# Kernel optimization log

Hardware: AMD Instinct MI355X
Metric: run time of the kernel (lower is better)

Reference implementation:

```python
import jax, jax.numpy as jnp
import numpy as np

# RootMLP architecture constants (data_size=16, width=64, depth=2, in=1, out=2*data)
DATA = 16
WIDTH = 64
OUT = 2 * DATA
LAYER_SHAPES = [(WIDTH, 1), (WIDTH,), (WIDTH, WIDTH), (WIDTH,), (OUT, WIDTH), (OUT,)]
SIZES = [int(np.prod(s)) for s in LAYER_SHAPES]
OFFS = np.cumsum([0] + SIZES).tolist()
LATENT = OFFS[-1]  # 6368


def _mlp_apply(thet, x):
    # Unflatten latent vector into MLP weights (order: W0,b0,W1,b1,W2,b2) and run it.
    W0 = thet[OFFS[0]:OFFS[1]].reshape(WIDTH, 1)
    b0 = thet[OFFS[1]:OFFS[2]]
    W1 = thet[OFFS[2]:OFFS[3]].reshape(WIDTH, WIDTH)
    b1 = thet[OFFS[3]:OFFS[4]]
    W2 = thet[OFFS[4]:OFFS[5]].reshape(OUT, WIDTH)
    b2 = thet[OFFS[5]:OFFS[6]]
    h = jax.nn.relu(W0 @ x + b0)
    h = jax.nn.relu(W1 @ h + b1)
    return W2 @ h + b2  # (OUT,)


def setup_inputs() -> dict:
    key = jax.random.key(0)
    k1, k2, k3, k4 = jax.random.split(key, 4)
    batch, T = 8, 64
    xs = jax.random.normal(k1, (batch, T, DATA), dtype=jnp.float32)
    ts = jnp.tile(jnp.linspace(0.0, 1.0, T, dtype=jnp.float32), (batch, 1))
    # A initialized as identity in the source; tiny noise keeps the recurrence non-trivial yet stable.
    A = jnp.eye(LATENT, dtype=jnp.float32) + 1e-4 * jax.random.normal(k2, (LATENT, LATENT), dtype=jnp.float32)
    B = 0.01 * jax.random.normal(k3, (LATENT, DATA + 1), dtype=jnp.float32)
    theta0 = 0.05 * jax.random.normal(k4, (LATENT,), dtype=jnp.float32)
    return {"xs": xs, "ts": ts, "A": A, "B": B, "theta0": theta0}


def reference(xs, ts, A, B, theta0):
    # xs: (batch, T, DATA); ts: (batch, T)
    def forward(xs_, ts_):
        def f(carry, inp):
            thet, x_hat, x_prev, t_prev = carry
            x_true, t_curr = inp  # x_true: (DATA,), t_curr: (1,)
            delta_t = t_curr - t_prev
            # forcing_prob = 1.0  ->  bernoulli(key, 1.0) is always True -> teacher forcing
            x_t = x_true
            # time_as_channel=True: prepend time to both current and previous inputs
            xt_c = jnp.concatenate([t_curr, x_t])
            xp_c = jnp.concatenate([t_prev, x_prev])
            thet_next = A @ thet + B @ (xt_c - xp_c)
            root_in = t_curr + delta_t  # (1,)
            out = _mlp_apply(thet_next, root_in)  # (2*DATA,)
            mean = jnp.tanh(out[:DATA])
            std = jax.nn.softplus(jnp.tanh(out[DATA:]))  # apply_tanh_uncertainty=True
            x_next = jnp.concatenate([mean, std])
            # carry update per source: new x_hat = mean, new x_prev = old x_hat
            return (thet_next, mean, x_hat, t_curr), x_next

        init = (theta0, xs_[0], xs_[0], -ts_[1:2])
        _, ys = jax.lax.scan(f, init, (xs_, ts_[:, None]))
        return ys  # (T, 2*DATA)

    return jax.vmap(forward)(xs, ts)
```

## Files before the change

kernel.cpp:

```cpp
#include <hip/hip_runtime.h>
#include <hip/hip_bf16.h>
#include <cmath>

#define LATENT 6368
#define TSTEPS 64
#define NDATA 16
#define NPANEL 398
#define KSPLIT 8
#define NCHUNK 199
#define CPS 25
#define NTILE (NPANEL*KSPLIT)
#define KBLK 796
#define AGENT __HIP_MEMORY_SCOPE_AGENT

typedef __attribute__((ext_vector_type(8))) short short8v;
typedef __attribute__((ext_vector_type(4))) float floatx4;

__device__ __forceinline__ unsigned short f2bf(float x) {
    union { float f; unsigned u; } c; c.f = x;
    unsigned r = (c.u + 0x7FFFu + ((c.u >> 16) & 1u)) >> 16;
    return (unsigned short)r;
}
__device__ __forceinline__ float bf2f(unsigned short h) {
    union { unsigned u; float f; } c; c.u = ((unsigned)h) << 16; return c.f;
}

__device__ __forceinline__ unsigned long long ld64c(const void* p) {
    return __hip_atomic_load((const unsigned long long*)p, __ATOMIC_RELAXED, AGENT);
}
__device__ __forceinline__ short8v ldT16c(const unsigned short* p) {
    union { short8v v; unsigned long long q[2]; } r;
    r.q[0] = ld64c(p);
    r.q[1] = ld64c(p + 4);
    return r.v;
}
__device__ __forceinline__ float ldfc(const float* p) {
    return __hip_atomic_load(p, __ATOMIC_RELAXED, AGENT);
}
__device__ __forceinline__ void stfc(float* p, float v) {
    __hip_atomic_store(p, v, __ATOMIC_RELAXED, AGENT);
}
__device__ __forceinline__ void stu16c(unsigned short* p, unsigned short v) {
    __hip_atomic_store(p, v, __ATOMIC_RELAXED, AGENT);
}

__global__ __launch_bounds__(64) void row_scale(const float* __restrict__ A,
                                                float* __restrict__ S) {
    int row = blockIdx.x;
    int lane = threadIdx.x;
    const float* Ar = A + (size_t)row * LATENT;
    float m = 0.f;
    for (int i = 0; i < 25; ++i) {
        int idx = i * 256 + lane * 4;
        if (idx + 4 <= LATENT) {
            float4 v = *reinterpret_cast<const float4*>(Ar + idx);
            float a0 = v.x - (idx + 0 == row ? 1.f : 0.f);
            float a1 = v.y - (idx + 1 == row ? 1.f : 0.f);
            float a2 = v.z - (idx + 2 == row ? 1.f : 0.f);
            float a3 = v.w - (idx + 3 == row ? 1.f : 0.f);
            m = fmaxf(m, fmaxf(fmaxf(fabsf(a0), fabsf(a1)), fmaxf(fabsf(a2), fabsf(a3))));
        }
    }
#pragma unroll
    for (int o = 32; o; o >>= 1) m = fmaxf(m, __shfl_xor(m, o, 64));
    if (lane == 0) S[row] = fmaxf(m, 1e-30f) * (1.0f / 32767.0f);
}

__global__ __launch_bounds__(256) void convert_Eq(const float* __restrict__ A,
                                                  const float* __restrict__ S,
                                                  short* __restrict__ Eq,
                                                  int total) {
    int t = blockIdx.x * 256 + threadIdx.x;
    if (t >= total) return;
    int row = t / KBLK;
    int kb  = t - row * KBLK;
    const float4* src = reinterpret_cast<const float4*>(A + (size_t)row * LATENT + kb * 8);
    float4 v0 = src[0];
    float4 v1 = src[1];
    float v[8] = {v0.x, v0.y, v0.z, v0.w, v1.x, v1.y, v1.z, v1.w};
    int jd = row - kb * 8;
    if (jd >= 0 && jd < 8) v[jd] -= 1.0f;
    float inv = 1.0f / S[row];
    union { short8v s; short q[8]; } o;
#pragma unroll
    for (int j = 0; j < 8; ++j) {
        float qf = rintf(v[j] * inv);
        qf = fminf(fmaxf(qf, -32767.f), 32767.f);
        o.q[j] = (short)qf;
    }
    int p = row >> 4, rowl = row & 15, c = kb >> 2, kgrp = kb & 3;
    int lane = kgrp * 16 + rowl;
    *reinterpret_cast<short8v*>(Eq + ((size_t)(p * NCHUNK + c)) * 512 + lane * 8) = o.s;
}

__global__ __launch_bounds__(256) void init_theta(const float* __restrict__ th0,
                                                  float* __restrict__ T0,
                                                  unsigned short* __restrict__ TTA) {
    int r = blockIdx.x * blockDim.x + threadIdx.x;
    if (r >= LATENT) return;
    float v = th0[r];
#pragma unroll
    for (int b = 0; b < 8; ++b) T0[r * 8 + b] = v;
    unsigned short hb = f2bf(v);
    unsigned short lb = f2bf(v - bf2f(hb));
#pragma unroll
    for (int n = 0; n < 8; ++n) {
        TTA[n * LATENT + r] = hb;
        TTA[(n + 8) * LATENT + r] = lb;
    }
}

__device__ void mlp_batch(const float* __restrict__ Tcur, const float* __restrict__ ts,
                          float* __restrict__ mwrite, float* __restrict__ ys,
                          int i, int b, int lane) {
    float tc = ts[b * TSTEPS + i];
    float tp = (i == 0) ? -ts[b * TSTEPS + 1] : ts[b * TSTEPS + i - 1];
    float rin = 2.f * tc - tp;
    float h0 = fmaxf(Tcur[(size_t)lane * 8 + b] * rin + Tcur[(size_t)(64 + lane) * 8 + b], 0.f);
    float h1 = Tcur[(size_t)(4224 + lane) * 8 + b];
#pragma unroll 8
    for (int k = 0; k < 64; ++k)
        h1 += Tcur[(size_t)(128 + lane * 64 + k) * 8 + b] * __shfl(h0, k, 64);
    h1 = fmaxf(h1, 0.f);
    float o = 0.f;
    if (lane < 32) o = Tcur[(size_t)(6336 + lane) * 8 + b];
#pragma unroll 8
    for (int k = 0; k < 64; ++k) {
        float hk = __shfl(h1, k, 64);
        if (lane < 32) o += Tcur[(size_t)(4288 + lane * 64 + k) * 8 + b] * hk;
    }
    if (lane < 32) {
        float z = tanhf(o);
        float res;
        if (lane < 16) { res = z; mwrite[b * NDATA + lane] = z; }
        else           { res = log1pf(expf(z)); }
        ys[(size_t)b * (TSTEPS * 32) + (size_t)i * 32 + lane] = res;
    }
}

__device__ void mlp_batch_coh(const float* __restrict__ Tcur, const float* __restrict__ ts,
                              float* __restrict__ mwrite, float* __restrict__ ys,
                              int i, int b, int lane) {
    float tc = ts[b * TSTEPS + i];
    float tp = (i == 0) ? -ts[b * TSTEPS + 1] : ts[b * TSTEPS + i - 1];
    float rin = 2.f * tc - tp;
    float h0 = fmaxf(ldfc(&Tcur[(size_t)lane * 8 + b]) * rin
                     + ldfc(&Tcur[(size_t)(64 + lane) * 8 + b]), 0.f);
    float h1 = ldfc(&Tcur[(size_t)(4224 + lane) * 8 + b]);
#pragma unroll 8
    for (int k = 0; k < 64; ++k)
        h1 += ldfc(&Tcur[(size_t)(128 + lane * 64 + k) * 8 + b]) * __shfl(h0, k, 64);
    h1 = fmaxf(h1, 0.f);
    float o = 0.f;
    if (lane < 32) o = ldfc(&Tcur[(size_t)(6336 + lane) * 8 + b]);
#pragma unroll 8
    for (int k = 0; k < 64; ++k) {
        float hk = __shfl(h1, k, 64);
        if (lane < 32) o += ldfc(&Tcur[(size_t)(4288 + lane * 64 + k) * 8 + b]) * hk;
    }
    if (lane < 32) {
        float z = tanhf(o);
        float res;
        if (lane < 16) { res = z; stfc(&mwrite[b * NDATA + lane], z); }
        else           { res = log1pf(expf(z)); }
        ys[(size_t)b * (TSTEPS * 32) + (size_t)i * 32 + lane] = res;
    }
}

__device__ __forceinline__ void gsync2(unsigned* grpCnt, unsigned* superCnt,
                                       unsigned* gEpoch, unsigned iter) {
    asm volatile("s_waitcnt vmcnt(0)" ::: "memory");
    __syncthreads();
    if (threadIdx.x == 0) {
        unsigned g = blockIdx.x & 15u;
        unsigned gsz = (g < 8u) ? 13u : 12u;
        unsigned v = __hip_atomic_fetch_add(&grpCnt[g * 32], 1u, __ATOMIC_RELAXED, AGENT);
        if (v == iter * gsz - 1u) {
            unsigned w = __hip_atomic_fetch_add(superCnt, 1u, __ATOMIC_RELAXED, AGENT);
            if (w == iter * 16u - 1u) {
#pragma unroll
                for (int i2 = 0; i2 < 16; ++i2)
                    __hip_atomic_store(&gEpoch[i2 * 32], iter, __ATOMIC_RELAXED, AGENT);
            }
        }
        while (__hip_atomic_load(&gEpoch[g * 32], __ATOMIC_RELAXED, AGENT) < iter)
            __builtin_amdgcn_s_sleep(4);
    }
    __syncthreads();
}

#define COMP(EV, TP) do {                                                       \
    union { short8v sv; unsigned short us[8]; } EHu, ELu;                       \
    _Pragma("unroll")                                                           \
    for (int j = 0; j < 8; ++j) {                                               \
        int q = (EV)[j];                                                        \
        union { float f; unsigned u; } ch, cl;                                  \
        ch.f = (float)(q >> 8);                                                 \
        cl.f = (float)(q & 255);                                                \
        EHu.us[j] = (unsigned short)(ch.u >> 16);                               \
        ELu.us[j] = (unsigned short)(cl.u >> 16);                               \
    }                                                                           \
    acc1 = __builtin_amdgcn_mfma_f32_16x16x32_bf16(EHu.sv, (TP), acc1, 0, 0, 0);\
    acc2 = __builtin_amdgcn_mfma_f32_16x16x32_bf16(ELu.sv, (TP), acc2, 0, 0, 0);\
} while (0)

#define LDE(P)  (*reinterpret_cast<const short8v*>(P))

__global__ __launch_bounds__(1024, 4) void persistent5(
    const short* __restrict__ Eq, const float* __restrict__ S,
    float* __restrict__ T0buf, float* __restrict__ T1buf,
    unsigned short* __restrict__ TTA, unsigned short* __restrict__ TTB,
    float* __restrict__ mb,
    const float* __restrict__ Bmat, const float* __restrict__ xs,
    const float* __restrict__ ts, float* __restrict__ ys,
    unsigned* grpCnt, unsigned* superCnt, unsigned* gEpoch)
{
    __shared__ float red[16][16][16];
    __shared__ float ush[17][8];
    int tid = threadIdx.x, blk = blockIdx.x;
    int wave = tid >> 6, lane = tid & 63;
    int rowl = lane & 15, kgrp = lane >> 4;
    int panel = blk * 2 + (wave >> 3);
    int w8 = wave & 7;
    int cs = w8 * 25;
    int ce = (w8 < 7) ? cs + 25 : NCHUNK;
    unsigned iter = 0;
    for (int s = 0; s < TSTEPS; ++s) {
        const float* Tc = (s & 1) ? T1buf : T0buf;
        float* Tn       = (s & 1) ? T0buf : T1buf;
        const unsigned short* TTc = (s & 1) ? TTB : TTA;
        unsigned short* TTn       = (s & 1) ? TTA : TTB;
        float* mwrite = mb + (s & 1) * 128;
        const float* mread = mb + ((s & 1) ^ 1) * 128;
        if (blk < 199) {
            if (tid < 136) {
                int b = tid & 7, j = tid >> 3;
                float tc = ts[b * TSTEPS + s];
                float tp = (s == 0) ? -ts[b * TSTEPS + 1] : ts[b * TSTEPS + s - 1];
                float val;
                if (j == 0) val = tc - tp;
                else {
                    int d = j - 1;
                    float xp = (s < 2) ? xs[(b * TSTEPS) * NDATA + d]
                                       : ldfc(&mread[b * NDATA + d]);
                    val = xs[(b * TSTEPS + s) * NDATA + d] - xp;
                }
                ush[j][b] = val;
            }
            floatx4 acc1 = {0.f, 0.f, 0.f, 0.f};
            floatx4 acc2 = {0.f, 0.f, 0.f, 0.f};
            const short* ep = Eq + ((size_t)(panel * NCHUNK + cs)) * 512 + lane * 8;
            const unsigned short* tq = TTc + (size_t)rowl * LATENT + kgrp * 8 + (size_t)cs * 32;
            short8v e0 = LDE(ep),        e1 = LDE(ep + 512),
                    e2 = LDE(ep + 1024), e3 = LDE(ep + 1536);
            short8v t0 = ldT16c(tq),      t1 = ldT16c(tq + 32),
                    t2 = ldT16c(tq + 64), t3 = ldT16c(tq + 96);
            int c = cs;
            for (; c + 8 <= ce; c += 4) {
                COMP(e0, t0); e0 = LDE(ep + 2048); t0 = ldT16c(tq + 128);
                COMP(e1, t1); e1 = LDE(ep + 2560); t1 = ldT16c(tq + 160);
                COMP(e2, t2); e2 = LDE(ep + 3072); t2 = ldT16c(tq + 192);
                COMP(e3, t3); e3 = LDE(ep + 3584); t3 = ldT16c(tq + 224);
                ep += 2048; tq += 128;
            }
            COMP(e0, t0); COMP(e1, t1); COMP(e2, t2); COMP(e3, t3);
            for (int k2 = 4; c + k2 < ce; ++k2) {
                e0 = LDE(ep + k2 * 512); t0 = ldT16c(tq + k2 * 32);
                COMP(e0, t0);
            }
#pragma unroll
            for (int r = 0; r < 4; ++r)
                red[wave][kgrp * 4 + r][rowl] = 256.f * acc1[r] + acc2[r];
            __syncthreads();
            if (tid < 256) {
                int m32 = tid >> 3, n = tid & 7;
                int ph = m32 >> 4, m = m32 & 15;
                float sum = 0.f;
#pragma unroll
                for (int w = 0; w < 8; ++w)
                    sum += red[ph * 8 + w][m][n] + red[ph * 8 + w][m][n + 8];
                int r = blk * 32 + m32;
                float val = ldfc(&Tc[r * 8 + n]) + S[r] * sum;
                const float* Brow = Bmat + r * 17;
#pragma unroll
                for (int j = 0; j < 17; ++j) val += Brow[j] * ush[j][n];
                stfc(&Tn[r * 8 + n], val);
                unsigned short hb = f2bf(val);
                stu16c(&TTn[n * LATENT + r], hb);
                stu16c(&TTn[(n + 8) * LATENT + r], f2bf(val - bf2f(hb)));
            }
        } else {
            if (s >= 1 && wave < 8)
                mlp_batch_coh(Tc, ts, mwrite, ys, s - 1, wave, lane);
        }
        ++iter; gsync2(grpCnt, superCnt, gEpoch, iter);
    }
    if (blk == 199 && wave < 8)
        mlp_batch_coh(T0buf, ts, mb, ys, TSTEPS - 1, wave, lane);
}

template<bool USE_E>
__global__ __launch_bounds__(128) void partial_kernel(
    const short* __restrict__ Eq, const float* __restrict__ S,
    const float* __restrict__ Af,
    const unsigned short* __restrict__ TTc,
    float* __restrict__ P)
{
    int blk = blockIdx.x;
    int p  = blk >> 3;
    int si = blk & 7;
    int tid = threadIdx.x;
    int wave = tid >> 6;
    int lane = tid & 63;
    int rowl = lane & 15;
    int kgrp = lane >> 4;
    int row = p * 16 + rowl;
    int c0 = si * CPS;
    int c1 = c0 + CPS; if (c1 > NCHUNK) c1 = NCHUNK;
    int nch = c1 - c0;
    int half = (nch + 1) >> 1;
    int csw = c0 + wave * half;
    int cew = csw + half; if (cew > c1) cew = c1;
    floatx4 acc1 = {0.f, 0.f, 0.f, 0.f};
    floatx4 acc2 = {0.f, 0.f, 0.f, 0.f};
    for (int c = csw; c < cew; ++c) {
        int k = c * 32 + kgrp * 8;
        short8v ehf, elf;
        if (USE_E) {
            short8v ev = *reinterpret_cast<const short8v*>(
                Eq + ((size_t)(p * NCHUNK + c)) * 512 + lane * 8);
            union { short8v sv; unsigned short us[8]; } EH, EL;
#pragma unroll
            for (int j = 0; j < 8; ++j) {
                int q = ev[j];
                union { float f; unsigned u; } ch2, cl2;
                ch2.f = (float)(q >> 8);
                cl2.f = (float)(q & 255);
                EH.us[j] = (unsigned short)(ch2.u >> 16);
                EL.us[j] = (unsigned short)(cl2.u >> 16);
            }
            ehf = EH.sv; elf = EL.sv;
        } else {
            const float* ap = Af + (size_t)row * LATENT + k;
            float v[8];
#pragma unroll
            for (int j = 0; j < 8; ++j) v[j] = ap[j];
            int jd = row - k;
            if (jd >= 0 && jd < 8) v[jd] -= 1.0f;
            union { short8v sv; unsigned short us[8]; } ch, cl;
#pragma unroll
            for (int j = 0; j < 8; ++j) {
                unsigned short hb = f2bf(v[j]);
                ch.us[j] = hb;
                cl.us[j] = f2bf(v[j] - bf2f(hb));
            }
            ehf = ch.sv; elf = cl.sv;
        }
        short8v tpf = *reinterpret_cast<const short8v*>(TTc + (size_t)rowl * LATENT + k);
        acc1 = __builtin_amdgcn_mfma_f32_16x16x32_bf16(ehf, tpf, acc1, 0, 0, 0);
        acc2 = __builtin_amdgcn_mfma_f32_16x16x32_bf16(elf, tpf, acc2, 0, 0, 0);
    }
    __shared__ float red[2][16][16];
#pragma unroll
    for (int r = 0; r < 4; ++r)
        red[wave][kgrp * 4 + r][rowl] = USE_E ? (256.f * acc1[r] + acc2[r])
                                              : (acc1[r] + acc2[r]);
    __syncthreads();
    int nn = tid & 15;
    if (nn < 8) {
        for (int mm = tid >> 4; mm < 16; mm += 8) {
            float s2 = red[0][mm][nn] + red[0][mm][nn + 8]
                     + red[1][mm][nn] + red[1][mm][nn + 8];
            if (USE_E) s2 *= S[p * 16 + mm];
            P[((size_t)(p * 8 + si) * 16 + mm) * 8 + nn] = s2;
        }
    }
}

__global__ __launch_bounds__(256) void combine_kernel(
    const float* __restrict__ P,
    const float* __restrict__ Tcur,
    float* __restrict__ Tnxt,
    unsigned short* __restrict__ TTn,
    const float* __restrict__ Bmat,
    const float* __restrict__ xs,
    const float* __restrict__ ts,
    const float* __restrict__ mread,
    float* __restrict__ mwrite,
    float* __restrict__ ys,
    int s, int do_matvec, int do_mlp)
{
    int tid = threadIdx.x;
    if ((int)blockIdx.x < 199) {
        if (!do_matvec) return;
        __shared__ float u[17][8];
        if (tid < 136) {
            int b = tid & 7;
            int j = tid >> 3;
            float tc = ts[b * TSTEPS + s];
            float tp = (s == 0) ? -ts[b * TSTEPS + 1] : ts[b * TSTEPS + s - 1];
            float val;
            if (j == 0) val = tc - tp;
            else {
                int d = j - 1;
                float xp = (s < 2) ? xs[(b * TSTEPS) * NDATA + d] : mread[b * NDATA + d];
                val = xs[(b * TSTEPS + s) * NDATA + d] - xp;
            }
            u[j][b] = val;
        }
        __syncthreads();
        int idx = blockIdx.x * 256 + tid;
        int r = idx >> 3;
        int n = idx & 7;
        int pp = r >> 4, mm = r & 15;
        const float* Pb = P + ((size_t)pp * 8) * 128 + mm * 8 + n;
        float sum = 0.f;
#pragma unroll
        for (int si = 0; si < KSPLIT; ++si) sum += Pb[si * 128];
        float val = Tcur[r * 8 + n] + sum;
        const float* Brow = Bmat + r * 17;
#pragma unroll
        for (int j = 0; j < 17; ++j) val += Brow[j] * u[j][n];
        Tnxt[r * 8 + n] = val;
        unsigned short hb = f2bf(val);
        TTn[n * LATENT + r] = hb;
        TTn[(n + 8) * LATENT + r] = f2bf(val - bf2f(hb));
    } else {
        if (!do_mlp) return;
        int w = tid >> 6, lane = tid & 63;
        for (int it = 0; it < 2; ++it)
            mlp_batch(Tcur, ts, mwrite, ys, s - 1, w * 2 + it, lane);
    }
}

extern "C" void kernel_launch(void* const* d_in, const int* in_sizes, int n_in,
                              void* d_out, int out_size, void* d_ws, size_t ws_size,
                              hipStream_t stream) {
    const float* xs  = (const float*)d_in[0];
    const float* ts  = (const float*)d_in[1];
    const float* A   = (const float*)d_in[2];
    const float* Bm  = (const float*)d_in[3];
    const float* th0 = (const float*)d_in[4];
    float* ys = (float*)d_out;

    char* ws = (char*)d_ws;
    size_t off = 0;
    auto alloc = [&](size_t bytes) {
        void* p = ws + off;
        off += (bytes + 255) & ~(size_t)255;
        return p;
    };
    float* T0 = (float*)alloc((size_t)LATENT * 8 * sizeof(float));
    float* T1 = (float*)alloc((size_t)LATENT * 8 * sizeof(float));
    unsigned short* TTA = (unsigned short*)alloc((size_t)16 * LATENT * 2);
    unsigned short* TTB = (unsigned short*)alloc((size_t)16 * LATENT * 2);
    float* mb = (float*)alloc(2 * 8 * 16 * sizeof(float));
    float* P  = (float*)alloc((size_t)NTILE * 128 * sizeof(float));
    float* S  = (float*)alloc((size_t)LATENT * sizeof(float));
    unsigned* bar = (unsigned*)alloc(8192);
    unsigned* grpCnt   = bar;
    unsigned* superCnt = bar + 512;
    unsigned* gEpoch   = bar + 544;
    size_t Ebytes = (size_t)NPANEL * NCHUNK * 512 * 2;
    bool useE = (off + Ebytes + 512) <= ws_size;
    short* Eq = nullptr;
    if (useE) {
        Eq = (short*)alloc(Ebytes);
        row_scale<<<dim3(LATENT), dim3(64), 0, stream>>>(A, S);
        int nthr = LATENT * KBLK;
        convert_Eq<<<dim3((nthr + 255) / 256), dim3(256), 0, stream>>>(A, S, Eq, nthr);
    }
    init_theta<<<dim3((LATENT + 255) / 256), dim3(256), 0, stream>>>(th0, T0, TTA);

    hipError_t coop = hipErrorUnknown;
    if (useE) {
        hipMemsetAsync(bar, 0, 8192, stream);
        void* kargs[] = {
            (void*)&Eq, (void*)&S, (void*)&T0, (void*)&T1,
            (void*)&TTA, (void*)&TTB, (void*)&mb, (void*)&Bm, (void*)&xs,
            (void*)&ts, (void*)&ys, (void*)&grpCnt, (void*)&superCnt, (void*)&gEpoch };
        coop = hipLaunchCooperativeKernel((void*)persistent5,
                                          dim3(200), dim3(1024), kargs, 0, stream);
    }
    if (coop != hipSuccess) {
        float* T[2] = {T0, T1};
        unsigned short* TT[2] = {TTA, TTB};
        for (int s = 0; s <= TSTEPS; ++s) {
            int cur = s & 1, nxt = cur ^ 1;
            float* mwrite = mb + (s & 1) * 128;
            float* mread  = mb + ((s & 1) ^ 1) * 128;
            int dmv = (s < TSTEPS) ? 1 : 0;
            int dml = (s >= 1) ? 1 : 0;
            if (dmv) {
                if (useE)
                    partial_kernel<true><<<dim3(NTILE), dim3(128), 0, stream>>>(
                        Eq, S, A, TT[cur], P);
                else
                    partial_kernel<false><<<dim3(NTILE), dim3(128), 0, stream>>>(
                        Eq, S, A, TT[cur], P);
            }
            combine_kernel<<<dim3(200), dim3(256), 0, stream>>>(
                P, T[cur], T[nxt], TT[nxt],
                Bm, xs, ts, mread, mwrite, ys, s, dmv, dml);
        }
    }
    (void)in_sizes; (void)n_in; (void)out_size;
}
```

Baseline: 2.410 ms.

## Share theta fragments across both panels per wave and use nontemporal theta loads

Each wave now processes both panels of a block over a smaller K-chunk range, so one loaded theta fragment feeds four MFMAs instead of two, halving theta load traffic per MFMA. The K split across waves changes from 8 to 16 ways and the reduction buffer doubles to hold two panels. Theta loads switch from agent-scope atomic 64-bit loads to nontemporal vector loads, with init writes made atomic, which relies on nontemporal loads seeing other blocks' writes after the grid barrier. The trade-off is more accumulator registers and a longer LDS reduction.

```diff
diff --git a/kernel.cpp b/kernel.cpp
--- a/kernel.cpp
+++ b/kernel.cpp
@@ -25,15 +25,6 @@
     union { unsigned u; float f; } c; c.u = ((unsigned)h) << 16; return c.f;
 }
 
-__device__ __forceinline__ unsigned long long ld64c(const void* p) {
-    return __hip_atomic_load((const unsigned long long*)p, __ATOMIC_RELAXED, AGENT);
-}
-__device__ __forceinline__ short8v ldT16c(const unsigned short* p) {
-    union { short8v v; unsigned long long q[2]; } r;
-    r.q[0] = ld64c(p);
-    r.q[1] = ld64c(p + 4);
-    return r.v;
-}
 __device__ __forceinline__ float ldfc(const float* p) {
     return __hip_atomic_load(p, __ATOMIC_RELAXED, AGENT);
 }
@@ -105,8 +96,8 @@
     unsigned short lb = f2bf(v - bf2f(hb));
 #pragma unroll
     for (int n = 0; n < 8; ++n) {
-        TTA[n * LATENT + r] = hb;
-        TTA[(n + 8) * LATENT + r] = lb;
+        stu16c(&TTA[n * LATENT + r], hb);
+        stu16c(&TTA[(n + 8) * LATENT + r], lb);
     }
 }
 
@@ -189,24 +180,27 @@
     __syncthreads();
 }
 
-#define COMP(EV, TP) do {                                                       \
-    union { short8v sv; unsigned short us[8]; } EHu, ELu;                       \
-    _Pragma("unroll")                                                           \
-    for (int j = 0; j < 8; ++j) {                                               \
-        int q = (EV)[j];                                                        \
-        union { float f; unsigned u; } ch, cl;                                  \
-        ch.f = (float)(q >> 8);                                                 \
-        cl.f = (float)(q & 255);                                                \
-        EHu.us[j] = (unsigned short)(ch.u >> 16);                               \
-        ELu.us[j] = (unsigned short)(cl.u >> 16);                               \
-    }                                                                           \
-    acc1 = __builtin_amdgcn_mfma_f32_16x16x32_bf16(EHu.sv, (TP), acc1, 0, 0, 0);\
-    acc2 = __builtin_amdgcn_mfma_f32_16x16x32_bf16(ELu.sv, (TP), acc2, 0, 0, 0);\
+#define COMP2(EA, EB, TP) do {                                                    \
+    union { short8v sv; unsigned short us[8]; } HA, LA, HB, LB;                   \
+    _Pragma("unroll")                                                             \
+    for (int j = 0; j < 8; ++j) {                                                 \
+        int qa = (EA)[j], qb = (EB)[j];                                           \
+        union { float f; unsigned u; } x0, x1, x2, x3;                            \
+        x0.f = (float)(qa >> 8);  HA.us[j] = (unsigned short)(x0.u >> 16);        \
+        x1.f = (float)(qa & 255); LA.us[j] = (unsigned short)(x1.u >> 16);        \
+        x2.f = (float)(qb >> 8);  HB.us[j] = (unsigned short)(x2.u >> 16);        \
+        x3.f = (float)(qb & 255); LB.us[j] = (unsigned short)(x3.u >> 16);        \
+    }                                                                             \
+    acc1A = __builtin_amdgcn_mfma_f32_16x16x32_bf16(HA.sv, (TP), acc1A, 0, 0, 0); \
+    acc2A = __builtin_amdgcn_mfma_f32_16x16x32_bf16(LA.sv, (TP), acc2A, 0, 0, 0); \
+    acc1B = __builtin_amdgcn_mfma_f32_16x16x32_bf16(HB.sv, (TP), acc1B, 0, 0, 0); \
+    acc2B = __builtin_amdgcn_mfma_f32_16x16x32_bf16(LB.sv, (TP), acc2B, 0, 0, 0); \
 } while (0)
 
 #define LDE(P)  (*reinterpret_cast<const short8v*>(P))
-
-__global__ __launch_bounds__(1024, 4) void persistent5(
+#define LDNT(P) (__builtin_nontemporal_load(reinterpret_cast<const short8v*>(P)))
+
+__global__ __launch_bounds__(1024, 4) void persistent6(
     const short* __restrict__ Eq, const float* __restrict__ S,
     float* __restrict__ T0buf, float* __restrict__ T1buf,
     unsigned short* __restrict__ TTA, unsigned short* __restrict__ TTB,
@@ -215,15 +209,14 @@
     const float* __restrict__ ts, float* __restrict__ ys,
     unsigned* grpCnt, unsigned* superCnt, unsigned* gEpoch)
 {
-    __shared__ float red[16][16][16];
+    __shared__ float red[16][2][16][16];
     __shared__ float ush[17][8];
     int tid = threadIdx.x, blk = blockIdx.x;
     int wave = tid >> 6, lane = tid & 63;
     int rowl = lane & 15, kgrp = lane >> 4;
-    int panel = blk * 2 + (wave >> 3);
-    int w8 = wave & 7;
-    int cs = w8 * 25;
-    int ce = (w8 < 7) ? cs + 25 : NCHUNK;
+    int cs = (wave < 7) ? wave * 13 : 91 + (wave - 7) * 12;
+    int nch = (wave < 7) ? 13 : 12;
+    int panelA = blk * 2;
     unsigned iter = 0;
     for (int s = 0; s < TSTEPS; ++s) {
         const float* Tc = (s & 1) ? T1buf : T0buf;
@@ -247,38 +240,43 @@
                 }
                 ush[j][b] = val;
             }
-            floatx4 acc1 = {0.f, 0.f, 0.f, 0.f};
-            floatx4 acc2 = {0.f, 0.f, 0.f, 0.f};
-            const short* ep = Eq + ((size_t)(panel * NCHUNK + cs)) * 512 + lane * 8;
+            floatx4 acc1A = {0.f,0.f,0.f,0.f}, acc2A = {0.f,0.f,0.f,0.f};
+            floatx4 acc1B = {0.f,0.f,0.f,0.f}, acc2B = {0.f,0.f,0.f,0.f};
+            const short* epA = Eq + ((size_t)(panelA * NCHUNK + cs)) * 512 + lane * 8;
+            const short* epB = epA + (size_t)NCHUNK * 512;
             const unsigned short* tq = TTc + (size_t)rowl * LATENT + kgrp * 8 + (size_t)cs * 32;
-            short8v e0 = LDE(ep),        e1 = LDE(ep + 512),
-                    e2 = LDE(ep + 1024), e3 = LDE(ep + 1536);
-            short8v t0 = ldT16c(tq),      t1 = ldT16c(tq + 32),
-                    t2 = ldT16c(tq + 64), t3 = ldT16c(tq + 96);
-            int c = cs;
-            for (; c + 8 <= ce; c += 4) {
-                COMP(e0, t0); e0 = LDE(ep + 2048); t0 = ldT16c(tq + 128);
-                COMP(e1, t1); e1 = LDE(ep + 2560); t1 = ldT16c(tq + 160);
-                COMP(e2, t2); e2 = LDE(ep + 3072); t2 = ldT16c(tq + 192);
-                COMP(e3, t3); e3 = LDE(ep + 3584); t3 = ldT16c(tq + 224);
-                ep += 2048; tq += 128;
-            }
-            COMP(e0, t0); COMP(e1, t1); COMP(e2, t2); COMP(e3, t3);
-            for (int k2 = 4; c + k2 < ce; ++k2) {
-                e0 = LDE(ep + k2 * 512); t0 = ldT16c(tq + k2 * 32);
-                COMP(e0, t0);
-            }
-#pragma unroll
-            for (int r = 0; r < 4; ++r)
-                red[wave][kgrp * 4 + r][rowl] = 256.f * acc1[r] + acc2[r];
+            short8v a0 = LDE(epA),        a1 = LDE(epA + 512),
+                    a2 = LDE(epA + 1024), a3 = LDE(epA + 1536);
+            short8v b0 = LDE(epB),        b1 = LDE(epB + 512),
+                    b2 = LDE(epB + 1024), b3 = LDE(epB + 1536);
+            short8v t0 = LDNT(tq),        t1 = LDNT(tq + 32),
+                    t2 = LDNT(tq + 64),   t3 = LDNT(tq + 96);
+            int c = 0;
+            for (; c + 8 <= nch; c += 4) {
+                COMP2(a0, b0, t0); a0 = LDE(epA + 2048); b0 = LDE(epB + 2048); t0 = LDNT(tq + 128);
+                COMP2(a1, b1, t1); a1 = LDE(epA + 2560); b1 = LDE(epB + 2560); t1 = LDNT(tq + 160);
+                COMP2(a2, b2, t2); a2 = LDE(epA + 3072); b2 = LDE(epB + 3072); t2 = LDNT(tq + 192);
+                COMP2(a3, b3, t3); a3 = LDE(epA + 3584); b3 = LDE(epB + 3584); t3 = LDNT(tq + 224);
+                epA += 2048; epB += 2048; tq += 128;
+            }
+            COMP2(a0, b0, t0); COMP2(a1, b1, t1); COMP2(a2, b2, t2); COMP2(a3, b3, t3);
+            for (int k2 = 4; c + k2 < nch; ++k2) {
+                a0 = LDE(epA + k2 * 512); b0 = LDE(epB + k2 * 512); t0 = LDNT(tq + k2 * 32);
+                COMP2(a0, b0, t0);
+            }
+#pragma unroll
+            for (int r = 0; r < 4; ++r) {
+                red[wave][0][kgrp * 4 + r][rowl] = 256.f * acc1A[r] + acc2A[r];
+                red[wave][1][kgrp * 4 + r][rowl] = 256.f * acc1B[r] + acc2B[r];
+            }
             __syncthreads();
             if (tid < 256) {
                 int m32 = tid >> 3, n = tid & 7;
                 int ph = m32 >> 4, m = m32 & 15;
                 float sum = 0.f;
 #pragma unroll
-                for (int w = 0; w < 8; ++w)
-                    sum += red[ph * 8 + w][m][n] + red[ph * 8 + w][m][n + 8];
+                for (int w = 0; w < 16; ++w)
+                    sum += red[w][ph][m][n] + red[w][ph][m][n + 8];
                 int r = blk * 32 + m32;
                 float val = ldfc(&Tc[r * 8 + n]) + S[r] * sum;
                 const float* Brow = Bmat + r * 17;
@@ -479,7 +477,7 @@
             (void*)&Eq, (void*)&S, (void*)&T0, (void*)&T1,
             (void*)&TTA, (void*)&TTB, (void*)&mb, (void*)&Bm, (void*)&xs,
             (void*)&ts, (void*)&ys, (void*)&grpCnt, (void*)&superCnt, (void*)&gEpoch };
-        coop = hipLaunchCooperativeKernel((void*)persistent5,
+        coop = hipLaunchCooperativeKernel((void*)persistent6,
                                           dim3(200), dim3(1024), kargs, 0, stream);
     }
     if (coop != hipSuccess) {
```

New measurement: 2.568 ms. 6.5% more time.
